# Performance work log

Hardware: AMD Instinct MI355X
Metric: run time of the kernel (lower is better)

## Reference

```python
import jax, jax.numpy as jnp
import numpy as np

S, T, C, L_GNN, L_TF, H = 8, 16, 128, 3, 2, 4
B = 512
FF = 4 * C
EPS = 1e-5


def setup_inputs() -> dict:
    key = jax.random.key(0)
    ks = jax.random.split(key, 24)
    w = lambda k, shape: jax.random.normal(k, shape, jnp.float32) * 0.05
    inp = {}
    inp["xx"] = jax.random.randint(ks[0], (B, T, S, S, S), 0, 3, dtype=jnp.int32)
    inp["ss"] = jax.random.uniform(ks[1], (B, 1), jnp.float32)
    # DynamicGNNv2 params
    inp["Win"] = w(ks[2], (C, 5)); inp["b_in"] = w(ks[3], (C,))
    inp["Wl"] = w(ks[4], (L_GNN, C, C)); inp["bl"] = w(ks[5], (L_GNN, C))   # SAGEConv lin_l (neighbors)
    inp["Wr"] = w(ks[6], (L_GNN, C, C))                                      # SAGEConv lin_r (root, no bias)
    inp["ln_g"] = jnp.ones((C,), jnp.float32); inp["ln_b"] = jnp.zeros((C,), jnp.float32)  # shared LayerNorm
    # TransformerEncoder params (norm_first, relu, dropout=0 at eval)
    inp["Wqkv"] = w(ks[7], (L_TF, 3 * C, C)); inp["bqkv"] = w(ks[8], (L_TF, 3 * C))
    inp["Wo"] = w(ks[9], (L_TF, C, C)); inp["bo"] = w(ks[10], (L_TF, C))
    inp["ln1_g"] = jnp.ones((L_TF, C), jnp.float32); inp["ln1_b"] = jnp.zeros((L_TF, C), jnp.float32)
    inp["ln2_g"] = jnp.ones((L_TF, C), jnp.float32); inp["ln2_b"] = jnp.zeros((L_TF, C), jnp.float32)
    inp["W1"] = w(ks[11], (L_TF, FF, C)); inp["b1"] = w(ks[12], (L_TF, FF))
    inp["W2"] = w(ks[13], (L_TF, C, FF)); inp["b2"] = w(ks[14], (L_TF, C))
    inp["Wact"] = w(ks[15], (C, S ** 3)); inp["bact"] = w(ks[16], (C,))
    inp["Wsc"] = w(ks[17], (C, 1)); inp["bsc"] = w(ks[18], (C,))
    return inp


def layernorm(x, g, b):
    mu = x.mean(-1, keepdims=True)
    var = ((x - mu) ** 2).mean(-1, keepdims=True)
    return (x - mu) * jax.lax.rsqrt(var + EPS) * g + b


def reference(xx, ss, Win, b_in, Wl, bl, Wr, ln_g, ln_b, Wqkv, bqkv, Wo, bo,
              ln1_g, ln1_b, ln2_g, ln2_b, W1, b1, W2, b2, Wact, bact, Wsc, bsc):
    Bc = xx.shape[0]
    S3 = S ** 3
    frame0 = xx[:, 0].reshape(Bc, S3).astype(jnp.float32)            # (B,S^3)
    m = (frame0 != 0).astype(jnp.float32)                            # active-node mask
    grid = jnp.arange(S3)
    i, j, k = grid // (S * S), (grid // S) % S, grid % S
    coord = jnp.stack([i, j, k], -1).astype(jnp.float32) / (S - 1)   # (S^3,3)
    feat = jnp.concatenate([
        jnp.broadcast_to(coord, (Bc, S3, 3)),
        (frame0 / 2.0)[..., None],
        jnp.broadcast_to((ss / S)[:, None, :], (Bc, S3, 1)),
    ], -1)                                                            # (B,S^3,5)
    x = feat @ Win.T + b_in                                           # lin_in
    mm = m[..., None]
    n = m.sum(-1, keepdims=True)[..., None]                           # nodes per graph (B,1,1)
    for l in range(L_GNN):
        # complete graph (no self loops): mean over neighbors = (sum_active - self)/(N-1)
        s = (x * mm).sum(1, keepdims=True)                            # (B,1,C)
        neigh = jnp.where(n > 1, (s - x) / jnp.maximum(n - 1.0, 1.0), 0.0)
        h = neigh @ Wl[l].T + bl[l] + x @ Wr[l].T                     # SAGEConv
        x = layernorm(jax.nn.relu(h), ln_g, ln_b)
    full = x * mm                                                     # scatter-fill into dense (B,S^3,C)
    # pooling matmul: mean over each i/j/k slice -> (B,3S,C)
    poolW = jnp.concatenate([
        (i[None, :] == jnp.arange(S)[:, None]).astype(jnp.float32),
        (j[None, :] == jnp.arange(S)[:, None]).astype(jnp.float32),
        (k[None, :] == jnp.arange(S)[:, None]).astype(jnp.float32),
    ], 0)                                                             # (3S,S^3)
    gnn_emb = jnp.einsum('ps,bsc->bpc', poolW, full) / poolW.sum(1)[None, :, None]
    # transformer over past actions
    a = xx[:, 1:].reshape(Bc, T - 1, S3).astype(jnp.float32) @ Wact.T + bact
    Hd = C // H
    scale = 1.0 / np.sqrt(Hd).astype(np.float32)
    split_heads = lambda t: t.reshape(Bc, -1, H, Hd).transpose(0, 2, 1, 3)
    for l in range(L_TF):
        h1 = layernorm(a, ln1_g[l], ln1_b[l])
        q, kk, v = jnp.split(h1 @ Wqkv[l].T + bqkv[l], 3, axis=-1)
        q, kk, v = split_heads(q), split_heads(kk), split_heads(v)
        att = jax.nn.softmax(jnp.einsum('bhqd,bhkd->bhqk', q, kk) * scale, -1)
        o = jnp.einsum('bhqk,bhkd->bhqd', att, v).transpose(0, 2, 1, 3).reshape(Bc, -1, C)
        a = a + (o @ Wo[l].T + bo[l])
        h2 = layernorm(a, ln2_g[l], ln2_b[l])
        a = a + (jax.nn.relu(h2 @ W1[l].T + b1[l]) @ W2[l].T + b2[l])
    act_emb = a.mean(1)                                               # (B,C)
    mv_emb = jax.nn.relu(ss @ Wsc.T + bsc)                            # (B,C)
    return jnp.concatenate([gnn_emb, act_emb[:, None], mv_emb[:, None]], 1)  # (B,3S+2,C)
```

## Files before the change

kernel.cpp:

```cpp
#include <hip/hip_runtime.h>
#include <hip/hip_bf16.h>
#include <string.h>

typedef __hip_bfloat16 bf16;
typedef __attribute__((ext_vector_type(8))) short short8;
typedef __attribute__((ext_vector_type(4))) float f32x4;

#define Bsz 512
#define S3  512
#define Tsz 16
#define Cc  128
#define TT  15
#define XP  136
#define EPSv 1e-5f

__device__ __forceinline__ float u2f(unsigned short u) {
    return __uint_as_float(((unsigned)u) << 16);
}
__device__ __forceinline__ float ulo(unsigned u) { return __uint_as_float(u << 16); }
__device__ __forceinline__ float uhi(unsigned u) { return __uint_as_float(u & 0xffff0000u); }
__device__ __forceinline__ unsigned short f2bu(float v) {
    bf16 h = __float2bfloat16(v);
    unsigned short u; memcpy(&u, &h, 2); return u;
}
__device__ __forceinline__ unsigned short bfr16(float a) {
    unsigned u = __float_as_uint(a);
    u = u + 0x7fffu + ((u >> 16) & 1u);
    return (unsigned short)(u >> 16);
}
__device__ __forceinline__ unsigned fpack2(float a, float b) {
    unsigned r;
    asm("v_cvt_pk_bf16_f32 %0, %1, %2" : "=v"(r) : "v"(a), "v"(b));
    return r;
}
__device__ __forceinline__ float dot4(float4 a, float4 b) {
    return a.x*b.x + a.y*b.y + a.z*b.z + a.w*b.w;
}


__global__ __launch_bounds__(256) void k_tpack(const float* __restrict__ src,
                                               float* __restrict__ dst,
                                               int NR, int NK)
{
    __shared__ float tile[32][33];
    int k0 = blockIdx.x * 32, r0 = blockIdx.y * 32;
    int lr = threadIdx.x >> 5, lk = threadIdx.x & 31;
    for (int i = lr; i < 32; i += 8)
        tile[i][lk] = src[(size_t)(r0 + i) * NK + k0 + lk];
    __syncthreads();
    int c = threadIdx.x & 31, k4 = threadIdx.x >> 5;
    float4 v;
    v.x = tile[c][k4 * 4 + 0]; v.y = tile[c][k4 * 4 + 1];
    v.z = tile[c][k4 * 4 + 2]; v.w = tile[c][k4 * 4 + 3];
    ((float4*)dst)[(size_t)(k0 / 4 + k4) * NR + r0 + c] = v;
}

__global__ __launch_bounds__(256) void k_cvt5(
    const float* __restrict__ s0, const float* __restrict__ s1,
    const float* __restrict__ s2, const float* __restrict__ s3,
    const float* __restrict__ s4, ushort* __restrict__ dst)
{
    int i = blockIdx.x * 256 + threadIdx.x;
    if (i >= 114688) return;
    const float* src; int rel;
    if (i < 16384)      { src = s0; rel = i; }
    else if (i < 40960) { src = s1; rel = i - 16384; }
    else if (i < 49152) { src = s2; rel = i - 40960; }
    else if (i < 81920) { src = s3; rel = i - 49152; }
    else                { src = s4; rel = i - 81920; }
    float4 v = ((const float4*)src)[rel];
    ushort4 o;
    o.x = f2bu(v.x); o.y = f2bu(v.y); o.z = f2bu(v.z); o.w = f2bu(v.w);
    ((ushort4*)dst)[i] = o;
}

__global__ __launch_bounds__(256) void k_wpack(
    const float* __restrict__ Wl, const float* __restrict__ Wr,
    ushort* __restrict__ WB)
{
    int l = blockIdx.x, w = blockIdx.y;
    const float* src = (w == 0 ? Wl : Wr) + l * 16384;
    ushort* dst = WB + (size_t)(l * 2 + w) * 32 * 512;
    for (int item = threadIdx.x; item < 2048; item += 256) {
        int f = item >> 6, lane = item & 63;
        int t = f >> 2, ks = f & 3, ml = lane & 15, q = lane >> 4;
        int n = t * 16 + ml;
        const float* sA = src + n * 128 + 32 * ks + q * 4;
        const float* sB = sA + 16;
        float4 a = *(const float4*)sA;
        float4 b = *(const float4*)sB;
        ushort4 o0, o1;
        o0.x = f2bu(a.x); o0.y = f2bu(b.x); o0.z = f2bu(a.y); o0.w = f2bu(b.y);
        o1.x = f2bu(a.z); o1.y = f2bu(b.z); o1.z = f2bu(a.w); o1.w = f2bu(b.w);
        ushort* dp = dst + (size_t)f * 512 + lane * 8;
        *(ushort4*)dp = o0;
        *(ushort4*)(dp + 4) = o1;
    }
}

__global__ __launch_bounds__(1024) void k_torso(
    const int* __restrict__ xx, const float* __restrict__ ss,
    const float* __restrict__ Win, const float* __restrict__ b_in,
    const ushort* __restrict__ WB,
    const float4* __restrict__ WlP, const float* __restrict__ blv,
    const float* __restrict__ lng, const float* __restrict__ lnb,
    float* __restrict__ out)
{
    __shared__ ushort X[512 * XP];
    __shared__ ushort Ds[16 * 512];
    __shared__ ushort mCu[512];
    __shared__ float  ssc[128];
    __shared__ float  sbase[128];
    __shared__ float  gln[128], bln[128];
    __shared__ float  scnt[8];
    __shared__ float  invS;

    int b = blockIdx.x, tid = threadIdx.x;
    int wv = tid >> 6, lane = tid & 63;
    int ml = lane & 15, quad = lane >> 4;

    int*   fC   = (int*)Ds;
    float* sred = (float*)(Ds + 4096);

    const int* x0 = xx + (size_t)b * Tsz * S3;
    if (tid < 512) {
        int f0 = x0[tid];
        fC[tid] = f0;
        mCu[tid] = (f0 != 0) ? (ushort)0x3F80 : (ushort)0;
        unsigned long long bal = __ballot(f0 != 0);
        if (lane == 0) scnt[wv] = (float)__popcll(bal);
    }
    if (tid < 128) { gln[tid] = lng[tid]; bln[tid] = lnb[tid]; }
    __syncthreads();

    {
        int cp = lane;
        int co0 = 32 * (cp >> 4) + (cp & 15), co1 = co0 + 16;
        float f4c = ss[b] * (1.0f / 8.0f);
        float a0 = Win[co0*5+0], a1 = Win[co0*5+1], a2 = Win[co0*5+2], a3 = Win[co0*5+3];
        float c0 = Win[co1*5+0], c1 = Win[co1*5+1], c2 = Win[co1*5+2], c3 = Win[co1*5+3];
        float ba = b_in[co0] + f4c * Win[co0*5+4];
        float bc = b_in[co1] + f4c * Win[co1*5+4];
        float sp0 = 0.f, sp1 = 0.f;
        for (int node = wv; node < S3; node += 16) {
            int f0 = fC[node];
            float m = (f0 != 0) ? 1.f : 0.f;
            float ci = (float)(node >> 6) * (1.f / 7.f);
            float cj = (float)((node >> 3) & 7) * (1.f / 7.f);
            float ck = (float)(node & 7) * (1.f / 7.f);
            float ft = (float)f0 * 0.5f;
            float v0 = ba + ci * a0 + cj * a1 + ck * a2 + ft * a3;
            float v1 = bc + ci * c0 + cj * c1 + ck * c2 + ft * c3;
            ((unsigned*)(X + node * XP))[cp] = fpack2(v0, v1);
            sp0 += v0 * m; sp1 += v1 * m;
        }
        sred[wv * 128 + co0] = sp0;
        sred[wv * 128 + co1] = sp1;
    }
    __syncthreads();
    if (tid == 0) {
        float n = 0.f;
#pragma unroll
        for (int g = 0; g < 8; g++) n += scnt[g];
        invS = (n > 1.f) ? 1.f / (n - 1.f) : 0.f;
    }
    __syncthreads();
    if (tid < 128) {
        float s = 0.f;
#pragma unroll
        for (int g = 0; g < 16; g++) s += sred[g * 128 + tid];
        ssc[tid] = s * invS;
    }
    __syncthreads();
    {
        int part = tid >> 7, c = tid & 127;
        float a = 0.f;
#pragma unroll
        for (int k4 = part * 4; k4 < part * 4 + 4; k4++)
            a += dot4(*(const float4*)(ssc + k4 * 4), WlP[k4 * 384 + c]);
        sred[part * 128 + c] = a;
    }
    __syncthreads();
    if (tid < 128) {
        float a = blv[tid];
#pragma unroll
        for (int p = 0; p < 8; p++) a += sred[p * 128 + tid];
        sbase[tid] = a;
    }
    __syncthreads();

    float ninv = -invS;

#define D_BUILD(H)                                                            \
    {                                                                         \
        const ushort* wl = WB + ((size_t)(l * 2 + 0) * 32 + (H) * 16) * 512;  \
        const ushort* wr = WB + ((size_t)(l * 2 + 1) * 32 + (H) * 16) * 512;  \
        int g = tid;                                                          \
        uint4 ul = *(const uint4*)(wl + g * 8);                               \
        uint4 ur = *(const uint4*)(wr + g * 8);                               \
        uint4 d;                                                              \
        d.x = fpack2(fmaf(ninv, ulo(ul.x), ulo(ur.x)), fmaf(ninv, uhi(ul.x), uhi(ur.x))); \
        d.y = fpack2(fmaf(ninv, ulo(ul.y), ulo(ur.y)), fmaf(ninv, uhi(ul.y), uhi(ur.y))); \
        d.z = fpack2(fmaf(ninv, ulo(ul.z), ulo(ur.z)), fmaf(ninv, uhi(ul.z), uhi(ur.z))); \
        d.w = fpack2(fmaf(ninv, ulo(ul.w), ulo(ur.w)), fmaf(ninv, uhi(ul.w), uhi(ur.w))); \
        *(uint4*)(Ds + g * 8) = d;                                            \
    }

#define GEMM_HALF(OFF)                                                        \
    _Pragma("unroll")                                                         \
    for (int ks = 0; ks < 4; ks++) {                                          \
        short8 a0 = *(const short8*)(xr0 + ks * 32);                          \
        short8 a1 = *(const short8*)(xr1 + ks * 32);                          \
        short8 bg[4];                                                         \
        _Pragma("unroll")                                                     \
        for (int t = 0; t < 4; t++)                                           \
            bg[t] = *(const short8*)(Ds + (size_t)(t * 4 + ks) * 512 + lane * 8); \
        _Pragma("unroll")                                                     \
        for (int t = 0; t < 4; t++) {                                         \
            acc[(OFF) + t][0] = __builtin_amdgcn_mfma_f32_16x16x32_bf16(a0, bg[t], acc[(OFF) + t][0], 0, 0, 0); \
            acc[(OFF) + t][1] = __builtin_amdgcn_mfma_f32_16x16x32_bf16(a1, bg[t], acc[(OFF) + t][1], 0, 0, 0); \
        }                                                                     \
    }

    for (int l = 0; l < 3; l++) {
        bool last = (l == 2);
        float sp[8];
#pragma unroll
        for (int t = 0; t < 8; t++) sp[t] = 0.f;

        f32x4 acc[8][2];
#pragma unroll
        for (int t = 0; t < 8; t++)
#pragma unroll
            for (int mm = 0; mm < 2; mm++) acc[t][mm] = (f32x4){0.f, 0.f, 0.f, 0.f};

        const ushort* xr0 = X + (wv * 32 + ml) * XP + quad * 8;
        const ushort* xr1 = xr0 + 16 * XP;

        D_BUILD(0); __syncthreads(); GEMM_HALF(0); __syncthreads();
        D_BUILD(1); __syncthreads(); GEMM_HALF(4); __syncthreads();

        float bse[8], gg[8], be[8];
#pragma unroll
        for (int t = 0; t < 8; t++) {
            bse[t] = sbase[t * 16 + ml];
            gg[t]  = gln[t * 16 + ml];
            be[t]  = bln[t * 16 + ml];
        }
#pragma unroll
        for (int mm = 0; mm < 2; mm++) {
#pragma unroll
            for (int r = 0; r < 4; r++) {
                int row = wv * 32 + mm * 16 + quad * 4 + r;
                float s = 0.f, q = 0.f;
#pragma unroll
                for (int t = 0; t < 8; t++) {
                    float vv = fmaxf(acc[t][mm][r] + bse[t], 0.f);
                    acc[t][mm][r] = vv;
                    s += vv; q = fmaf(vv, vv, q);
                }
#pragma unroll
                for (int off = 1; off <= 8; off <<= 1) {
                    s += __shfl_xor(s, off, 64);
                    q += __shfl_xor(q, off, 64);
                }
                float mu = s * (1.f / 128.f);
                float rs = rsqrtf(q * (1.f / 128.f) - mu * mu + EPSv);
                float mrow = u2f(mCu[row]);
                unsigned* xr32 = (unsigned*)(X + row * XP);
                if (last) {
#pragma unroll
                    for (int t2 = 0; t2 < 4; t2++) {
                        float y0 = ((acc[2*t2][mm][r]   - mu) * rs * gg[2*t2]   + be[2*t2])   * mrow;
                        float y1 = ((acc[2*t2+1][mm][r] - mu) * rs * gg[2*t2+1] + be[2*t2+1]) * mrow;
                        xr32[t2 * 16 + ml] = fpack2(y0, y1);
                    }
                } else {
#pragma unroll
                    for (int t2 = 0; t2 < 4; t2++) {
                        float y0 = (acc[2*t2][mm][r]   - mu) * rs * gg[2*t2]   + be[2*t2];
                        float y1 = (acc[2*t2+1][mm][r] - mu) * rs * gg[2*t2+1] + be[2*t2+1];
                        sp[2*t2]   = fmaf(y0, mrow, sp[2*t2]);
                        sp[2*t2+1] = fmaf(y1, mrow, sp[2*t2+1]);
                        xr32[t2 * 16 + ml] = fpack2(y0, y1);
                    }
                }
            }
        }

        if (!last) {
#pragma unroll
            for (int t = 0; t < 8; t++) {
                sp[t] += __shfl_xor(sp[t], 16, 64);
                sp[t] += __shfl_xor(sp[t], 32, 64);
            }
            if (quad == 0) {
#pragma unroll
                for (int t = 0; t < 8; t++) sred[wv * 128 + t * 16 + ml] = sp[t];
            }
            __syncthreads();
            if (tid < 128) {
                float s = 0.f;
#pragma unroll
                for (int g = 0; g < 16; g++) s += sred[g * 128 + tid];
                ssc[tid] = s * invS;
            }
            __syncthreads();
            {
                int part = tid >> 7, c = tid & 127;
                float a = 0.f;
#pragma unroll
                for (int k4 = part * 4; k4 < part * 4 + 4; k4++)
                    a += dot4(*(const float4*)(ssc + k4 * 4), WlP[k4 * 384 + (l + 1) * 128 + c]);
                sred[part * 128 + c] = a;
            }
            __syncthreads();
            if (tid < 128) {
                float a = blv[(l + 1) * 128 + tid];
#pragma unroll
                for (int p = 0; p < 8; p++) a += sred[p * 128 + tid];
                sbase[tid] = a;
            }
            __syncthreads();
        }
    }
    __syncthreads();

    if (tid < 768) {
        int c4 = tid & 31, p = tid >> 5;
        int axis = p >> 3, idx = p & 7;
        float4 sum = {0.f, 0.f, 0.f, 0.f};
        for (int t = 0; t < 64; t++) {
            int node;
            if (axis == 0)      node = idx * 64 + t;
            else if (axis == 1) node = (t >> 3) * 64 + idx * 8 + (t & 7);
            else                node = t * 8 + idx;
            uint2 pk = *(const uint2*)(X + node * XP + c4 * 4);
            sum.x += ulo(pk.x);
            sum.y += uhi(pk.x);
            sum.z += ulo(pk.y);
            sum.w += uhi(pk.y);
        }
        int E0 = 32 * (c4 >> 3) + 2 * (c4 & 7);
        float* ob = out + (size_t)b * 26 * Cc + p * Cc;
        float2 lo = {sum.x * (1.f / 64.f), sum.z * (1.f / 64.f)};
        float2 hi = {sum.y * (1.f / 64.f), sum.w * (1.f / 64.f)};
        *(float2*)(ob + E0)      = lo;
        *(float2*)(ob + E0 + 16) = hi;
    }
}

__global__ __launch_bounds__(256) void k_tf3(
    const int* __restrict__ xx, const float* __restrict__ ss,
    const ushort* __restrict__ WactB, const float* __restrict__ bact,
    const ushort* __restrict__ WqkvB, const float* __restrict__ bqkv,
    const ushort* __restrict__ WoB, const float* __restrict__ bo,
    const float* __restrict__ ln1g, const float* __restrict__ ln1b,
    const float* __restrict__ ln2g, const float* __restrict__ ln2b,
    const ushort* __restrict__ W1B, const float* __restrict__ b1v,
    const ushort* __restrict__ W2B, const float* __restrict__ b2v,
    const float* __restrict__ Wsc, const float* __restrict__ bsc,
    float* __restrict__ out)
{
    __shared__ float  As[TT * 132];
    __shared__ ushort Qs[16 * 392];
    __shared__ ushort Ab[16 * 136];
    __shared__ ushort Hs[16 * 136];
    __shared__ ushort Fs[16 * 520];
    __shared__ float  Att[60 * 16];
    __shared__ float  mu_s[TT], rs_s[TT];

    int b = blockIdx.x, tid = threadIdx.x;
    int wv = tid >> 6, lane = tid & 63;
    int ml = lane & 15, quad = lane >> 4;

    const int* xa = xx + (size_t)b * Tsz * S3 + S3;
    {
        const int4* xa4 = (const int4*)xa;
        for (int i = tid; i < 1920; i += 256) {
            int4 v = xa4[i];
            int t = i >> 7, s = (i & 127) << 2;
            ushort4 o;
            o.x = bfr16((float)v.x); o.y = bfr16((float)v.y);
            o.z = bfr16((float)v.z); o.w = bfr16((float)v.w);
            *(ushort4*)(Fs + t * 520 + s) = o;
        }
    }
    __syncthreads();

    {
        f32x4 acc[2];
#pragma unroll
        for (int i = 0; i < 2; i++) acc[i] = (f32x4){0.f, 0.f, 0.f, 0.f};
        const ushort* ar = Fs + ml * 520 + quad * 8;
        for (int ks = 0; ks < 16; ks++) {
            short8 a = *(const short8*)(ar + ks * 32);
#pragma unroll
            for (int i = 0; i < 2; i++) {
                int n0 = (wv * 2 + i) * 16;
                short8 bfr = *(const short8*)(WactB + (size_t)(n0 + ml) * 512 + quad * 8 + ks * 32);
                acc[i] = __builtin_amdgcn_mfma_f32_16x16x32_bf16(a, bfr, acc[i], 0, 0, 0);
            }
        }
#pragma unroll
        for (int i = 0; i < 2; i++) {
            int col = (wv * 2 + i) * 16 + ml;
            float bb = bact[col];
#pragma unroll
            for (int r = 0; r < 4; r++) {
                int row = quad * 4 + r;
                if (row < TT) As[row * 132 + col] = acc[i][r] + bb;
            }
        }
    }
    __syncthreads();

    for (int l = 0; l < 2; l++) {
        const float* bq  = bqkv + l * 384;
        const float* bol = bo + l * 128;
        const float* g1  = ln1g + l * 128; const float* be1 = ln1b + l * 128;
        const float* g2  = ln2g + l * 128; const float* be2 = ln2b + l * 128;
        const float* b1l = b1v + l * 512;  const float* b2l = b2v + l * 128;

        for (int r = wv; r < TT; r += 4) {
            float2 v = *(const float2*)(As + r * 132 + lane * 2);
            float s = v.x + v.y, q = v.x * v.x + v.y * v.y;
            for (int off = 32; off; off >>= 1) {
                s += __shfl_xor(s, off, 64);
                q += __shfl_xor(q, off, 64);
            }
            if (lane == 0) {
                float mu = s * (1.f / 128.f);
                mu_s[r] = mu;
                rs_s[r] = rsqrtf(q * (1.f / 128.f) - mu * mu + EPSv);
            }
        }
        __syncthreads();
        for (int f = tid; f < TT * 64; f += 256) {
            int t = f >> 6, cp = f & 63;
            float mu = mu_s[t], rs = rs_s[t];
            float x0 = (As[t * 132 + 2 * cp]     - mu) * rs * g1[2 * cp]     + be1[2 * cp];
            float x1 = (As[t * 132 + 2 * cp + 1] - mu) * rs * g1[2 * cp + 1] + be1[2 * cp + 1];
            ((unsigned*)(Ab + t * 136))[cp] = fpack2(x0, x1);
        }
        __syncthreads();

        {
            short8 a[4];
            const ushort* ar = Ab + ml * 136 + quad * 8;
#pragma unroll
            for (int ks = 0; ks < 4; ks++) a[ks] = *(const short8*)(ar + ks * 32);
#pragma unroll
            for (int i = 0; i < 6; i++) {
                int n0 = (wv * 6 + i) * 16;
                f32x4 acc = (f32x4){0.f, 0.f, 0.f, 0.f};
                const ushort* wb = WqkvB + (size_t)(l * 384 + n0 + ml) * 128 + quad * 8;
#pragma unroll
                for (int ks = 0; ks < 4; ks++) {
                    short8 bfr = *(const short8*)(wb + ks * 32);
                    acc = __builtin_amdgcn_mfma_f32_16x16x32_bf16(a[ks], bfr, acc, 0, 0, 0);
                }
                int col = n0 + ml;
                float bb = bq[col];
#pragma unroll
                for (int r = 0; r < 4; r++) {
                    int row = quad * 4 + r;
                    if (row < TT) Qs[row * 392 + col] = bfr16(acc[r] + bb);
                }
            }
        }
        __syncthreads();

        if (tid < 240) {
            int pair = tid >> 2, part = tid & 3;
            int h = pair / 15, tq = pair % 15;
            const ushort* qp = Qs + tq * 392 + h * 32 + part * 8;
            float sc[TT];
#pragma unroll
            for (int tk = 0; tk < TT; tk++) {
                const ushort* kp = Qs + tk * 392 + 128 + h * 32 + part * 8;
                uint2 qa = *(const uint2*)(qp);
                uint2 qb = *(const uint2*)(qp + 4);
                uint2 ka = *(const uint2*)(kp);
                uint2 kb = *(const uint2*)(kp + 4);
                float d = ulo(qa.x) * ulo(ka.x) + uhi(qa.x) * uhi(ka.x)
                        + ulo(qa.y) * ulo(ka.y) + uhi(qa.y) * uhi(ka.y)
                        + ulo(qb.x) * ulo(kb.x) + uhi(qb.x) * uhi(kb.x)
                        + ulo(qb.y) * ulo(kb.y) + uhi(qb.y) * uhi(kb.y);
                d += __shfl_xor(d, 1, 64);
                d += __shfl_xor(d, 2, 64);
                sc[tk] = d * 0.17677669529663689f;
            }
            if (part == 0) {
                float mx = -1e30f;
#pragma unroll
                for (int tk = 0; tk < TT; tk++) mx = fmaxf(mx, sc[tk]);
                float sum = 0.f;
#pragma unroll
                for (int tk = 0; tk < TT; tk++) { float e = __expf(sc[tk] - mx); sc[tk] = e; sum += e; }
                float r = 1.f / sum;
#pragma unroll
                for (int tk = 0; tk < TT; tk++) Att[pair * 16 + tk] = sc[tk] * r;
            }
        }
        __syncthreads();

        for (int f = tid; f < TT * 64; f += 256) {
            int t = f >> 6, cp = f & 63;
            int h = cp >> 4;
            const float* ap = Att + (h * 15 + t) * 16;
            const ushort* vp = Qs + 256 + 2 * cp;
            float a0 = 0.f, a1 = 0.f;
#pragma unroll
            for (int tk = 0; tk < TT; tk++) {
                float w = ap[tk];
                unsigned pk = *(const unsigned*)(vp + tk * 392);
                a0 += w * ulo(pk);
                a1 += w * uhi(pk);
            }
            ((unsigned*)(Hs + t * 136))[cp] = fpack2(a0, a1);
        }
        __syncthreads();

        {
            short8 a[4];
            const ushort* ar = Hs + ml * 136 + quad * 8;
#pragma unroll
            for (int ks = 0; ks < 4; ks++) a[ks] = *(const short8*)(ar + ks * 32);
#pragma unroll
            for (int i = 0; i < 2; i++) {
                int n0 = (wv * 2 + i) * 16;
                f32x4 acc = (f32x4){0.f, 0.f, 0.f, 0.f};
                const ushort* wb = WoB + (size_t)(l * 128 + n0 + ml) * 128 + quad * 8;
#pragma unroll
                for (int ks = 0; ks < 4; ks++) {
                    short8 bfr = *(const short8*)(wb + ks * 32);
                    acc = __builtin_amdgcn_mfma_f32_16x16x32_bf16(a[ks], bfr, acc, 0, 0, 0);
                }
                int col = n0 + ml;
                float bb = bol[col];
#pragma unroll
                for (int r = 0; r < 4; r++) {
                    int row = quad * 4 + r;
                    if (row < TT) As[row * 132 + col] += acc[r] + bb;
                }
            }
        }
        __syncthreads();

        for (int r = wv; r < TT; r += 4) {
            float2 v = *(const float2*)(As + r * 132 + lane * 2);
            float s = v.x + v.y, q = v.x * v.x + v.y * v.y;
            for (int off = 32; off; off >>= 1) {
                s += __shfl_xor(s, off, 64);
                q += __shfl_xor(q, off, 64);
            }
            if (lane == 0) {
                float mu = s * (1.f / 128.f);
                mu_s[r] = mu;
                rs_s[r] = rsqrtf(q * (1.f / 128.f) - mu * mu + EPSv);
            }
        }
        __syncthreads();
        for (int f = tid; f < TT * 64; f += 256) {
            int t = f >> 6, cp = f & 63;
            float mu = mu_s[t], rs = rs_s[t];
            float x0 = (As[t * 132 + 2 * cp]     - mu) * rs * g2[2 * cp]     + be2[2 * cp];
            float x1 = (As[t * 132 + 2 * cp + 1] - mu) * rs * g2[2 * cp + 1] + be2[2 * cp + 1];
            ((unsigned*)(Ab + t * 136))[cp] = fpack2(x0, x1);
        }
        __syncthreads();

        {
            short8 a[4];
            const ushort* ar = Ab + ml * 136 + quad * 8;
#pragma unroll
            for (int ks = 0; ks < 4; ks++) a[ks] = *(const short8*)(ar + ks * 32);
#pragma unroll
            for (int i = 0; i < 8; i++) {
                int n0 = (wv * 8 + i) * 16;
                f32x4 acc = (f32x4){0.f, 0.f, 0.f, 0.f};
                const ushort* wb = W1B + (size_t)(l * 512 + n0 + ml) * 128 + quad * 8;
#pragma unroll
                for (int ks = 0; ks < 4; ks++) {
                    short8 bfr = *(const short8*)(wb + ks * 32);
                    acc = __builtin_amdgcn_mfma_f32_16x16x32_bf16(a[ks], bfr, acc, 0, 0, 0);
                }
                int col = n0 + ml;
                float bb = b1l[col];
#pragma unroll
                for (int r = 0; r < 4; r++) {
                    int row = quad * 4 + r;
                    if (row < TT) Fs[row * 520 + col] = bfr16(fmaxf(acc[r] + bb, 0.f));
                }
            }
        }
        __syncthreads();

        {
            f32x4 acc[2];
#pragma unroll
            for (int i = 0; i < 2; i++) acc[i] = (f32x4){0.f, 0.f, 0.f, 0.f};
            const ushort* ar = Fs + ml * 520 + quad * 8;
            for (int ks = 0; ks < 16; ks++) {
                short8 a = *(const short8*)(ar + ks * 32);
#pragma unroll
                for (int i = 0; i < 2; i++) {
                    int n0 = (wv * 2 + i) * 16;
                    short8 bfr = *(const short8*)(W2B + (size_t)(l * 128 + n0 + ml) * 512 + quad * 8 + ks * 32);
                    acc[i] = __builtin_amdgcn_mfma_f32_16x16x32_bf16(a, bfr, acc[i], 0, 0, 0);
                }
            }
#pragma unroll
            for (int i = 0; i < 2; i++) {
                int col = (wv * 2 + i) * 16 + ml;
                float bb = b2l[col];
#pragma unroll
                for (int r = 0; r < 4; r++) {
                    int row = quad * 4 + r;
                    if (row < TT) As[row * 132 + col] += acc[i][r] + bb;
                }
            }
        }
        __syncthreads();
    }

    if (tid < 128) {
        float s = 0.f;
#pragma unroll
        for (int t = 0; t < TT; t++) s += As[t * 132 + tid];
        out[(size_t)b * 26 * Cc + 24 * Cc + tid] = s * (1.f / 15.f);
    } else if (tid < 256) {
        int co = tid - 128;
        float v = ss[b] * Wsc[co] + bsc[co];
        out[(size_t)b * 26 * Cc + 25 * Cc + co] = fmaxf(v, 0.f);
    }
}

extern "C" void kernel_launch(void* const* d_in, const int* in_sizes, int n_in,
                              void* d_out, int out_size, void* d_ws, size_t ws_size,
                              hipStream_t stream)
{
    (void)in_sizes; (void)n_in; (void)out_size; (void)ws_size;
    const int*   xx   = (const int*)d_in[0];
    const float* ss   = (const float*)d_in[1];
    const float* Win  = (const float*)d_in[2];
    const float* b_in = (const float*)d_in[3];
    const float* Wl   = (const float*)d_in[4];
    const float* bl   = (const float*)d_in[5];
    const float* Wr   = (const float*)d_in[6];
    const float* lng  = (const float*)d_in[7];
    const float* lnb  = (const float*)d_in[8];
    const float* Wqkv = (const float*)d_in[9];
    const float* bqkv = (const float*)d_in[10];
    const float* Wo   = (const float*)d_in[11];
    const float* bo   = (const float*)d_in[12];
    const float* ln1g = (const float*)d_in[13];
    const float* ln1b = (const float*)d_in[14];
    const float* ln2g = (const float*)d_in[15];
    const float* ln2b = (const float*)d_in[16];
    const float* W1   = (const float*)d_in[17];
    const float* b1   = (const float*)d_in[18];
    const float* W2   = (const float*)d_in[19];
    const float* b2   = (const float*)d_in[20];
    const float* Wact = (const float*)d_in[21];
    const float* bact = (const float*)d_in[22];
    const float* Wsc  = (const float*)d_in[23];
    const float* bsc  = (const float*)d_in[24];
    float* out = (float*)d_out;

    char* ws = (char*)d_ws;
    size_t off = 0;
    float* WlT  = (float*)(ws + off); off += 384 * 128 * 4;
    ushort* WB    = (ushort*)(ws + off); off += (size_t)3 * 2 * 128 * 128 * 2;
    ushort* WactB = (ushort*)(ws + off); off += 128 * 512 * 2;
    ushort* WqkvB = (ushort*)(ws + off); off += 768 * 128 * 2;
    ushort* WoB   = (ushort*)(ws + off); off += 256 * 128 * 2;
    ushort* W1B   = (ushort*)(ws + off); off += 1024 * 128 * 2;
    ushort* W2B   = (ushort*)(ws + off); off += 256 * 512 * 2;

    k_tpack<<<dim3(4, 12), 256, 0, stream>>>(Wl, WlT, 384, 128);
    k_cvt5<<<448, 256, 0, stream>>>(Wact, Wqkv, Wo, W1, W2, WactB);
    k_wpack<<<dim3(3, 2), 256, 0, stream>>>(Wl, Wr, WB);

    k_torso<<<Bsz, 1024, 0, stream>>>(xx, ss, Win, b_in, WB,
                                      (const float4*)WlT, bl, lng, lnb, out);

    k_tf3<<<Bsz, 256, 0, stream>>>(xx, ss,
                                   WactB, bact, WqkvB, bqkv, WoB, bo,
                                   ln1g, ln1b, ln2g, ln2b,
                                   W1B, b1, W2B, b2,
                                   Wsc, bsc, out);
}
```

Before: 283.4 us.

## Double transformer kernel block to 512 threads and reload LN params in torso

The transformer kernel now launches 512 threads (8 waves) per batch element instead of 256, and each wave takes half as many MFMA output tiles in every GEMM stage (Wact, QKV, Wo, W1, W2) and in the layernorm and elementwise loops. The goal is more latency hiding and parallelism within each block. The cost is more threads competing for the same LDS footprint and more barrier participants. Separately, the torso kernel stops caching bias and LayerNorm gamma/beta in registers and reads them from shared memory at each use, which lowers register pressure at the price of extra LDS reads.

```diff
diff --git a/kernel.cpp b/kernel.cpp
--- a/kernel.cpp
+++ b/kernel.cpp
@@ -240,13 +240,6 @@
         D_BUILD(0); __syncthreads(); GEMM_HALF(0); __syncthreads();
         D_BUILD(1); __syncthreads(); GEMM_HALF(4); __syncthreads();
 
-        float bse[8], gg[8], be[8];
-#pragma unroll
-        for (int t = 0; t < 8; t++) {
-            bse[t] = sbase[t * 16 + ml];
-            gg[t]  = gln[t * 16 + ml];
-            be[t]  = bln[t * 16 + ml];
-        }
 #pragma unroll
         for (int mm = 0; mm < 2; mm++) {
 #pragma unroll
@@ -255,7 +248,7 @@
                 float s = 0.f, q = 0.f;
 #pragma unroll
                 for (int t = 0; t < 8; t++) {
-                    float vv = fmaxf(acc[t][mm][r] + bse[t], 0.f);
+                    float vv = fmaxf(acc[t][mm][r] + sbase[t * 16 + ml], 0.f);
                     acc[t][mm][r] = vv;
                     s += vv; q = fmaf(vv, vv, q);
                 }
@@ -271,15 +264,15 @@
                 if (last) {
 #pragma unroll
                     for (int t2 = 0; t2 < 4; t2++) {
-                        float y0 = ((acc[2*t2][mm][r]   - mu) * rs * gg[2*t2]   + be[2*t2])   * mrow;
-                        float y1 = ((acc[2*t2+1][mm][r] - mu) * rs * gg[2*t2+1] + be[2*t2+1]) * mrow;
+                        float y0 = ((acc[2*t2][mm][r]   - mu) * rs * gln[(2*t2)*16 + ml]   + bln[(2*t2)*16 + ml])   * mrow;
+                        float y1 = ((acc[2*t2+1][mm][r] - mu) * rs * gln[(2*t2+1)*16 + ml] + bln[(2*t2+1)*16 + ml]) * mrow;
                         xr32[t2 * 16 + ml] = fpack2(y0, y1);
                     }
                 } else {
 #pragma unroll
                     for (int t2 = 0; t2 < 4; t2++) {
-                        float y0 = (acc[2*t2][mm][r]   - mu) * rs * gg[2*t2]   + be[2*t2];
-                        float y1 = (acc[2*t2+1][mm][r] - mu) * rs * gg[2*t2+1] + be[2*t2+1];
+                        float y0 = (acc[2*t2][mm][r]   - mu) * rs * gln[(2*t2)*16 + ml]   + bln[(2*t2)*16 + ml];
+                        float y1 = (acc[2*t2+1][mm][r] - mu) * rs * gln[(2*t2+1)*16 + ml] + bln[(2*t2+1)*16 + ml];
                         sp[2*t2]   = fmaf(y0, mrow, sp[2*t2]);
                         sp[2*t2+1] = fmaf(y1, mrow, sp[2*t2+1]);
                         xr32[t2 * 16 + ml] = fpack2(y0, y1);
@@ -350,7 +343,7 @@
     }
 }
 
-__global__ __launch_bounds__(256) void k_tf3(
+__global__ __launch_bounds__(512) void k_tf3(
     const int* __restrict__ xx, const float* __restrict__ ss,
     const ushort* __restrict__ WactB, const float* __restrict__ bact,
     const ushort* __restrict__ WqkvB, const float* __restrict__ bqkv,
@@ -377,7 +370,7 @@
     const int* xa = xx + (size_t)b * Tsz * S3 + S3;
     {
         const int4* xa4 = (const int4*)xa;
-        for (int i = tid; i < 1920; i += 256) {
+        for (int i = tid; i < 1920; i += 512) {
             int4 v = xa4[i];
             int t = i >> 7, s = (i & 127) << 2;
             ushort4 o;
@@ -389,28 +382,20 @@
     __syncthreads();
 
     {
-        f32x4 acc[2];
-#pragma unroll
-        for (int i = 0; i < 2; i++) acc[i] = (f32x4){0.f, 0.f, 0.f, 0.f};
+        f32x4 acc = (f32x4){0.f, 0.f, 0.f, 0.f};
         const ushort* ar = Fs + ml * 520 + quad * 8;
+        const ushort* wb = WactB + (size_t)(wv * 16 + ml) * 512 + quad * 8;
         for (int ks = 0; ks < 16; ks++) {
-            short8 a = *(const short8*)(ar + ks * 32);
-#pragma unroll
-            for (int i = 0; i < 2; i++) {
-                int n0 = (wv * 2 + i) * 16;
-                short8 bfr = *(const short8*)(WactB + (size_t)(n0 + ml) * 512 + quad * 8 + ks * 32);
-                acc[i] = __builtin_amdgcn_mfma_f32_16x16x32_bf16(a, bfr, acc[i], 0, 0, 0);
-            }
-        }
-#pragma unroll
-        for (int i = 0; i < 2; i++) {
-            int col = (wv * 2 + i) * 16 + ml;
-            float bb = bact[col];
-#pragma unroll
-            for (int r = 0; r < 4; r++) {
-                int row = quad * 4 + r;
-                if (row < TT) As[row * 132 + col] = acc[i][r] + bb;
-            }
+            short8 a   = *(const short8*)(ar + ks * 32);
+            short8 bfr = *(const short8*)(wb + ks * 32);
+            acc = __builtin_amdgcn_mfma_f32_16x16x32_bf16(a, bfr, acc, 0, 0, 0);
+        }
+        int col = wv * 16 + ml;
+        float bb = bact[col];
+#pragma unroll
+        for (int r = 0; r < 4; r++) {
+            int row = quad * 4 + r;
+            if (row < TT) As[row * 132 + col] = acc[r] + bb;
         }
     }
     __syncthreads();
@@ -422,7 +407,7 @@
         const float* g2  = ln2g + l * 128; const float* be2 = ln2b + l * 128;
         const float* b1l = b1v + l * 512;  const float* b2l = b2v + l * 128;
 
-        for (int r = wv; r < TT; r += 4) {
+        for (int r = wv; r < TT; r += 8) {
             float2 v = *(const float2*)(As + r * 132 + lane * 2);
             float s = v.x + v.y, q = v.x * v.x + v.y * v.y;
             for (int off = 32; off; off >>= 1) {
@@ -436,7 +421,7 @@
             }
         }
         __syncthreads();
-        for (int f = tid; f < TT * 64; f += 256) {
+        for (int f = tid; f < TT * 64; f += 512) {
             int t = f >> 6, cp = f & 63;
             float mu = mu_s[t], rs = rs_s[t];
             float x0 = (As[t * 132 + 2 * cp]     - mu) * rs * g1[2 * cp]     + be1[2 * cp];
@@ -451,8 +436,8 @@
 #pragma unroll
             for (int ks = 0; ks < 4; ks++) a[ks] = *(const short8*)(ar + ks * 32);
 #pragma unroll
-            for (int i = 0; i < 6; i++) {
-                int n0 = (wv * 6 + i) * 16;
+            for (int i = 0; i < 3; i++) {
+                int n0 = (wv * 3 + i) * 16;
                 f32x4 acc = (f32x4){0.f, 0.f, 0.f, 0.f};
                 const ushort* wb = WqkvB + (size_t)(l * 384 + n0 + ml) * 128 + quad * 8;
 #pragma unroll
@@ -505,7 +490,7 @@
         }
         __syncthreads();
 
-        for (int f = tid; f < TT * 64; f += 256) {
+        for (int f = tid; f < TT * 64; f += 512) {
             int t = f >> 6, cp = f & 63;
             int h = cp >> 4;
             const float* ap = Att + (h * 15 + t) * 16;
@@ -527,28 +512,25 @@
             const ushort* ar = Hs + ml * 136 + quad * 8;
 #pragma unroll
             for (int ks = 0; ks < 4; ks++) a[ks] = *(const short8*)(ar + ks * 32);
-#pragma unroll
-            for (int i = 0; i < 2; i++) {
-                int n0 = (wv * 2 + i) * 16;
-                f32x4 acc = (f32x4){0.f, 0.f, 0.f, 0.f};
-                const ushort* wb = WoB + (size_t)(l * 128 + n0 + ml) * 128 + quad * 8;
-#pragma unroll
-                for (int ks = 0; ks < 4; ks++) {
-                    short8 bfr = *(const short8*)(wb + ks * 32);
-                    acc = __builtin_amdgcn_mfma_f32_16x16x32_bf16(a[ks], bfr, acc, 0, 0, 0);
-                }
-                int col = n0 + ml;
-                float bb = bol[col];
-#pragma unroll
-                for (int r = 0; r < 4; r++) {
-                    int row = quad * 4 + r;
-                    if (row < TT) As[row * 132 + col] += acc[r] + bb;
-                }
-            }
-        }
-        __syncthreads();
-
-        for (int r = wv; r < TT; r += 4) {
+            int n0 = wv * 16;
+            f32x4 acc = (f32x4){0.f, 0.f, 0.f, 0.f};
+            const ushort* wb = WoB + (size_t)(l * 128 + n0 + ml) * 128 + quad * 8;
+#pragma unroll
+            for (int ks = 0; ks < 4; ks++) {
+                short8 bfr = *(const short8*)(wb + ks * 32);
+                acc = __builtin_amdgcn_mfma_f32_16x16x32_bf16(a[ks], bfr, acc, 0, 0, 0);
+            }
+            int col = n0 + ml;
+            float bb = bol[col];
+#pragma unroll
+            for (int r = 0; r < 4; r++) {
+                int row = quad * 4 + r;
+                if (row < TT) As[row * 132 + col] += acc[r] + bb;
+            }
+        }
+        __syncthreads();
+
+        for (int r = wv; r < TT; r += 8) {
             float2 v = *(const float2*)(As + r * 132 + lane * 2);
             float s = v.x + v.y, q = v.x * v.x + v.y * v.y;
             for (int off = 32; off; off >>= 1) {
@@ -562,7 +544,7 @@
             }
         }
         __syncthreads();
-        for (int f = tid; f < TT * 64; f += 256) {
+        for (int f = tid; f < TT * 64; f += 512) {
             int t = f >> 6, cp = f & 63;
             float mu = mu_s[t], rs = rs_s[t];
             float x0 = (As[t * 132 + 2 * cp]     - mu) * rs * g2[2 * cp]     + be2[2 * cp];
@@ -577,8 +559,8 @@
 #pragma unroll
             for (int ks = 0; ks < 4; ks++) a[ks] = *(const short8*)(ar + ks * 32);
 #pragma unroll
-            for (int i = 0; i < 8; i++) {
-                int n0 = (wv * 8 + i) * 16;
+            for (int i = 0; i < 4; i++) {
+                int n0 = (wv * 4 + i) * 16;
                 f32x4 acc = (f32x4){0.f, 0.f, 0.f, 0.f};
                 const ushort* wb = W1B + (size_t)(l * 512 + n0 + ml) * 128 + quad * 8;
 #pragma unroll
@@ -598,28 +580,21 @@
         __syncthreads();
 
         {
-            f32x4 acc[2];
-#pragma unroll
-            for (int i = 0; i < 2; i++) acc[i] = (f32x4){0.f, 0.f, 0.f, 0.f};
+            f32x4 acc = (f32x4){0.f, 0.f, 0.f, 0.f};
             const ushort* ar = Fs + ml * 520 + quad * 8;
+            int n0 = wv * 16;
+            const ushort* wb = W2B + (size_t)(l * 128 + n0 + ml) * 512 + quad * 8;
             for (int ks = 0; ks < 16; ks++) {
-                short8 a = *(const short8*)(ar + ks * 32);
-#pragma unroll
-                for (int i = 0; i < 2; i++) {
-                    int n0 = (wv * 2 + i) * 16;
-                    short8 bfr = *(const short8*)(W2B + (size_t)(l * 128 + n0 + ml) * 512 + quad * 8 + ks * 32);
-                    acc[i] = __builtin_amdgcn_mfma_f32_16x16x32_bf16(a, bfr, acc[i], 0, 0, 0);
-                }
-            }
-#pragma unroll
-            for (int i = 0; i < 2; i++) {
-                int col = (wv * 2 + i) * 16 + ml;
-                float bb = b2l[col];
-#pragma unroll
-                for (int r = 0; r < 4; r++) {
-                    int row = quad * 4 + r;
-                    if (row < TT) As[row * 132 + col] += acc[i][r] + bb;
-                }
+                short8 a   = *(const short8*)(ar + ks * 32);
+                short8 bfr = *(const short8*)(wb + ks * 32);
+                acc = __builtin_amdgcn_mfma_f32_16x16x32_bf16(a, bfr, acc, 0, 0, 0);
+            }
+            int col = n0 + ml;
+            float bb = b2l[col];
+#pragma unroll
+            for (int r = 0; r < 4; r++) {
+                int row = quad * 4 + r;
+                if (row < TT) As[row * 132 + col] += acc[r] + bb;
             }
         }
         __syncthreads();
@@ -686,7 +661,7 @@
     k_torso<<<Bsz, 1024, 0, stream>>>(xx, ss, Win, b_in, WB,
                                       (const float4*)WlT, bl, lng, lnb, out);
 
-    k_tf3<<<Bsz, 256, 0, stream>>>(xx, ss,
+    k_tf3<<<Bsz, 512, 0, stream>>>(xx, ss,
                                    WactB, bact, WqkvB, bqkv, WoB, bo,
                                    ln1g, ln1b, ln2g, ln2b,
                                    W1B, b1, W2B, b2,
```

New measurement: 280.5 us. Within noise of the previous version (-1.0%).
